# Performance work log

Measured on AMD Instinct MI355X. Metric: run time of the kernel, lower is better.

## Reference

```python
import jax, jax.numpy as jnp
import numpy as np
from jax import lax

B, C, H, W = 32, 64, 56, 56
G = 4            # num_heads*2 with num_heads=2
SMK, K = 5, 7
C2 = C // 2
HEAD_DIM = C // G
SCALE = HEAD_DIM ** -0.5


def _bias_idx(k, h, w):
    # static replica of ContMix.generate_idx + apply_rpb index construction
    rpb_size = 2 * k - 1
    idx_h = np.arange(k)
    idx_w = np.arange(k)
    idx_k = (idx_h[:, None] * rpb_size + idx_w).reshape(-1)
    rep_h = np.ones(k, np.int64); rep_h[k // 2] = h - (k - 1)
    rep_w = np.ones(k, np.int64); rep_w[k // 2] = w - (k - 1)
    bias_hw = np.repeat(idx_h, rep_h)[:, None] * rpb_size + np.repeat(idx_w, rep_w)  # (h, w)
    bias_idx = (bias_hw[..., None] + idx_k).reshape(-1, k * k)[::-1]  # torch.flip dim 0
    return jnp.asarray(bias_idx.copy())

IDX1 = _bias_idx(SMK, H, W)
IDX2 = _bias_idx(K, H, W)


def setup_inputs() -> dict:
    key = jax.random.key(0)
    ks = jax.random.split(key, 18)
    r = lambda i, sh: jax.random.normal(ks[i], sh, jnp.float32)
    return dict(
        x=r(0, (B, C, H, W)),
        lepe_w=r(1, (C, 1, K, K)) * 0.1,
        lepe_b=r(2, (C,)) * 0.1,
        lepe_bn_s=1.0 + 0.1 * r(3, (C,)),
        lepe_bn_b=0.1 * r(4, (C,)),
        wq_w=r(5, (C2, C2)) * (C2 ** -0.5),
        wq_bn_s=1.0 + 0.1 * r(6, (C2,)),
        wq_bn_b=0.1 * r(7, (C2,)),
        wk_w=r(8, (C2, C2)) * (C2 ** -0.5),
        wk_bn_s=1.0 + 0.1 * r(9, (C2,)),
        wk_bn_b=0.1 * r(10, (C2,)),
        wp_w=r(11, (SMK * SMK + K * K, 49)) * (49 ** -0.5),
        wp_b=0.1 * r(12, (SMK * SMK + K * K,)),
        rpb1=0.02 * r(13, (G, 2 * SMK - 1, 2 * SMK - 1)),
        rpb2=0.02 * r(14, (G, 2 * K - 1, 2 * K - 1)),
        dy_w=r(15, (C, C)) * (C ** -0.5),
        dy_bn_s=1.0 + 0.1 * r(16, (C,)),
        dy_bn_b=0.1 * r(17, (C,)),
    )


def _per_ch(t):
    return t[None, :, None, None]


def _contmix(x, lepe_w, lepe_b, lepe_bn_s, lepe_bn_b, wq_w, wq_bn_s, wq_bn_b,
             wk_w, wk_bn_s, wk_bn_b, wp_w, wp_b, rpb1, rpb2, dy_w, dy_bn_s, dy_bn_b):
    # lepe: deploy-mode DilatedReparamBlock = depthwise 7x7 conv (+bias), then eval BN
    lepe = lax.conv_general_dilated(x, lepe_w, (1, 1), [(K // 2, K // 2)] * 2,
                                    feature_group_count=C)
    lepe = (lepe + _per_ch(lepe_b)) * _per_ch(lepe_bn_s) + _per_ch(lepe_bn_b)

    q, kf = jnp.split(x, 2, axis=1)                         # (B, C2, H, W) each
    q = jnp.einsum('oi,bihw->bohw', wq_w, q)                # weight_query 1x1 conv
    q = (q * _per_ch(wq_bn_s) + _per_ch(wq_bn_b)) * SCALE
    # weight_key: AdaptiveAvgPool2d(7) -> 1x1 conv -> BN (H,W divisible by 7)
    kp = kf.reshape(B, C2, 7, H // 7, 7, W // 7).mean(axis=(3, 5))
    kp = jnp.einsum('oi,bihw->bohw', wk_w, kp)
    kp = kp * _per_ch(wk_bn_s) + _per_ch(wk_bn_b)

    qg = q.reshape(B, G, C2 // G, H * W)                    # b g c n
    kg = kp.reshape(B, G, C2 // G, 49)                      # b g c l
    w = jnp.einsum('bgcn,bgcl->bgnl', qg, kg)               # (B, G, HW, 49)
    # weight_proj: 1x1 conv over the 49 pooled-context channels
    w = jnp.einsum('ml,bgnl->bgnm', wp_w, w) + wp_b         # (B, G, HW, 74)
    w = w.reshape(B, G, H, W, SMK * SMK + K * K)

    attn1 = w[..., :SMK * SMK]
    attn2 = w[..., SMK * SMK:]
    attn1 = attn1 + rpb1.reshape(G, -1)[:, IDX1].reshape(1, G, H, W, SMK * SMK)
    attn2 = attn2 + rpb2.reshape(G, -1)[:, IDX2].reshape(1, G, H, W, K * K)
    attn1 = jax.nn.softmax(attn1, axis=-1)
    attn2 = jax.nn.softmax(attn2, axis=-1)

    c = C // (2 * G)                                        # value head dim = 8
    v = x.reshape(B, 2, G, c, H, W)                         # 'b (m g c) h w'

    def dyn_mix(attn, val, k):
        # unfold + einsum: content-adaptive depthwise mixing
        p = lax.conv_general_dilated_patches(
            val.reshape(B, G * c, H, W), (k, k), (1, 1), [(k // 2, k // 2)] * 2,
            dimension_numbers=('NCHW', 'OIHW', 'NCHW'))
        p = p.reshape(B, G, c, k * k, H, W)                 # channel-major patch layout
        return jnp.einsum('bgckhw,bghwk->bgchw', p, attn)

    x1 = dyn_mix(attn1, v[:, 0], SMK)
    x2 = dyn_mix(attn2, v[:, 1], K)
    out = jnp.concatenate([x1, x2], axis=1).reshape(B, C, H, W)
    out = jnp.einsum('oi,bihw->bohw', dy_w, out)            # dyconv_proj 1x1 + BN
    out = out * _per_ch(dy_bn_s) + _per_ch(dy_bn_b)
    return out + lepe


def reference(x, lepe_w, lepe_b, lepe_bn_s, lepe_bn_b, wq_w, wq_bn_s, wq_bn_b,
              wk_w, wk_bn_s, wk_bn_b, wp_w, wp_b, rpb1, rpb2, dy_w, dy_bn_s, dy_bn_b):
    return _contmix(x, lepe_w, lepe_b, lepe_bn_s, lepe_bn_b, wq_w, wq_bn_s, wq_bn_b,
                    wk_w, wk_bn_s, wk_bn_b, wp_w, wp_b, rpb1, rpb2, dy_w, dy_bn_s, dy_bn_b)
```

## Files before the change

### kernel.cpp

```cpp
#include <hip/hip_runtime.h>

#define BB 32
#define CC 64
#define C2 32
#define HH 56
#define WW 56
#define HW 3136

__global__ __launch_bounds__(256) void lepe_k(const float* __restrict__ x,
                                              const float* __restrict__ wt,
                                              const float* __restrict__ b,
                                              const float* __restrict__ s,
                                              const float* __restrict__ bb,
                                              float* __restrict__ out) {
    const int t = blockIdx.x * 256 + threadIdx.x;
    const int q = t % 784;
    const int bc = t / 784;
    const int c = bc & 63;
    const int r = q / 14;
    const int c4 = (q % 14) * 4;
    const float* xp = x + (long)bc * HW;
    float acc0 = 0.f, acc1 = 0.f, acc2 = 0.f, acc3 = 0.f;
    #pragma unroll
    for (int i = 0; i < 7; ++i) {
        const int y = r + i - 3;
        if ((unsigned)y >= HH) continue;
        float w7[7];
        #pragma unroll
        for (int j = 0; j < 7; ++j) w7[j] = wt[c * 49 + i * 7 + j];
        const float4* row = reinterpret_cast<const float4*>(xp + y * WW + c4 - 4);
        float4 A = make_float4(0.f, 0.f, 0.f, 0.f);
        float4 Cv = make_float4(0.f, 0.f, 0.f, 0.f);
        if (c4 != 0) A = row[0];
        const float4 Bv = row[1];
        if (c4 != 52) Cv = row[2];
        const float w12[12] = {A.x, A.y, A.z, A.w, Bv.x, Bv.y, Bv.z, Bv.w, Cv.x, Cv.y, Cv.z, Cv.w};
        #pragma unroll
        for (int j = 0; j < 7; ++j) {
            acc0 = fmaf(w12[j + 1], w7[j], acc0);
            acc1 = fmaf(w12[j + 2], w7[j], acc1);
            acc2 = fmaf(w12[j + 3], w7[j], acc2);
            acc3 = fmaf(w12[j + 4], w7[j], acc3);
        }
    }
    const float bc_ = b[c], sc = s[c], bbc = bb[c];
    float* op = out + (long)bc * HW + r * WW + c4;
    op[0] = (acc0 + bc_) * sc + bbc;
    op[1] = (acc1 + bc_) * sc + bbc;
    op[2] = (acc2 + bc_) * sc + bbc;
    op[3] = (acc3 + bc_) * sc + bbc;
}

__global__ __launch_bounds__(256) void q_k(const float* __restrict__ x,
                                           const float* __restrict__ wq,
                                           const float* __restrict__ s,
                                           const float* __restrict__ bb,
                                           float* __restrict__ q) {
    __shared__ float wsm[32 * 32];
    const int b = blockIdx.y;
    const int tid = threadIdx.x;
    for (int i = tid; i < 1024; i += 256) wsm[(i & 31) * 32 + (i >> 5)] = wq[i];
    __syncthreads();
    const int n = blockIdx.x * 256 + tid;
    if (n >= HW) return;
    const float* xp = x + (long)b * CC * HW;
    float acc[32];
    #pragma unroll
    for (int o = 0; o < 32; ++o) acc[o] = 0.f;
    for (int i = 0; i < 32; ++i) {
        const float xv = xp[i * HW + n];
        #pragma unroll
        for (int o = 0; o < 32; ++o) acc[o] = fmaf(wsm[i * 32 + o], xv, acc[o]);
    }
    float* qp = q + (long)b * C2 * HW + n;
    #pragma unroll
    for (int o = 0; o < 32; ++o)
        qp[o * HW] = (acc[o] * s[o] + bb[o]) * 0.25f;
}

__global__ __launch_bounds__(256) void prep_k(const float* __restrict__ x,
                                              const float* __restrict__ wk,
                                              const float* __restrict__ wks,
                                              const float* __restrict__ wkb,
                                              const float* __restrict__ wp_w,
                                              float* __restrict__ WK) {
    __shared__ float p_s[32 * 49];
    __shared__ float kg_s[8 * 49];
    const int b = blockIdx.x >> 2;
    const int g = blockIdx.x & 3;
    const int tid = threadIdx.x;
    for (int idx = tid; idx < 1568; idx += 256) {
        const int i = idx / 49, l = idx % 49;
        const int py = l / 7, px = l % 7;
        const float4* xp4 = reinterpret_cast<const float4*>(
            x + ((long)(b * CC + 32 + i)) * HW + py * 8 * WW + px * 8);
        float4 sA = make_float4(0.f, 0.f, 0.f, 0.f);
        float4 sB = make_float4(0.f, 0.f, 0.f, 0.f);
        #pragma unroll
        for (int y = 0; y < 8; ++y) {
            const float4 a = xp4[y * 14];
            const float4 c = xp4[y * 14 + 1];
            sA.x += a.x; sA.y += a.y; sA.z += a.z; sA.w += a.w;
            sB.x += c.x; sB.y += c.y; sB.z += c.z; sB.w += c.w;
        }
        p_s[idx] = (sA.x + sA.y + sA.z + sA.w + sB.x + sB.y + sB.z + sB.w) * (1.f / 64.f);
    }
    __syncthreads();
    for (int idx = tid; idx < 392; idx += 256) {
        const int o8 = idx / 49, l = idx % 49;
        const int o = g * 8 + o8;
        float acc = 0.f;
        #pragma unroll
        for (int i = 0; i < 32; ++i) acc = fmaf(wk[o * 32 + i], p_s[i * 49 + l], acc);
        kg_s[idx] = acc * wks[o] + wkb[o];
    }
    __syncthreads();
    for (int idx = tid; idx < 640; idx += 256) {
        const int c = idx / 80, slot = idx % 80;
        float acc = 0.f;
        int m = -1;
        if (slot < 28) { if (slot < 25) m = slot; }
        else           { if (slot < 77) m = 25 + (slot - 28); }
        if (m >= 0) {
            const float* kp = kg_s + c * 49;
            #pragma unroll
            for (int l = 0; l < 49; ++l) acc = fmaf(wp_w[m * 49 + l], kp[l], acc);
        }
        const long base = (long)blockIdx.x * 640;
        if (slot < 28) WK[base + c * 28 + slot] = acc;
        else           WK[base + 224 + c * 52 + (slot - 28)] = acc;
    }
}

__global__ __launch_bounds__(256) void attnmix_k(const float* __restrict__ x,
                                                 const float* __restrict__ q,
                                                 const float* __restrict__ WK,
                                                 const float* __restrict__ wp_b,
                                                 const float* __restrict__ rpb1,
                                                 const float* __restrict__ rpb2,
                                                 float* __restrict__ mix) {
    __shared__ float WK1_s[8 * 28];
    __shared__ float WK2_s[8 * 52];
    __shared__ float wpb1_s[25];
    __shared__ float wpb2_s[49];
    __shared__ float rpb1_s[81];
    __shared__ float rpb2_s[169];
    const int tid = threadIdx.x;
    const int bg = blockIdx.y;
    const int g = bg & 3, b = bg >> 2;
    {
        const float* wkp = WK + (long)bg * 640;
        for (int i = tid; i < 224; i += 256) WK1_s[i] = wkp[i];
        for (int i = tid; i < 416; i += 256) WK2_s[i] = wkp[224 + i];
    }
    if (tid < 25) wpb1_s[tid] = wp_b[tid];
    if (tid >= 32 && tid < 81) wpb2_s[tid - 32] = wp_b[25 + tid - 32];
    if (tid < 81) rpb1_s[tid] = rpb1[g * 81 + tid];
    if (tid < 169) rpb2_s[tid] = rpb2[g * 169 + tid];
    __syncthreads();
    const int n = blockIdx.x * 256 + tid;
    if (n >= HW) return;

    const int ph = n / WW, pw = n % WW;
    const int yr = HH - 1 - ph, xr = WW - 1 - pw;

    float q8[8];
    #pragma unroll
    for (int c = 0; c < 8; ++c) q8[c] = q[((long)b * C2 + g * 8 + c) * HW + n];

    {
        float w1[25];
        #pragma unroll
        for (int m = 0; m < 25; ++m) w1[m] = wpb1_s[m];
        #pragma unroll
        for (int c = 0; c < 8; ++c) {
            const float qv = q8[c];
            #pragma unroll
            for (int m = 0; m < 25; ++m) w1[m] = fmaf(qv, WK1_s[c * 28 + m], w1[m]);
        }
        const int rh5 = yr < 2 ? yr : (yr > 53 ? yr - 51 : 2);
        const int rw5 = xr < 2 ? xr : (xr > 53 ? xr - 51 : 2);
        #pragma unroll
        for (int i = 0; i < 5; ++i)
            #pragma unroll
            for (int j = 0; j < 5; ++j)
                w1[i * 5 + j] += rpb1_s[(rh5 + i) * 9 + (rw5 + j)];
        float mx = -1e30f;
        #pragma unroll
        for (int m = 0; m < 25; ++m) mx = fmaxf(mx, w1[m]);
        float sm = 0.f;
        #pragma unroll
        for (int m = 0; m < 25; ++m) { w1[m] = __expf(w1[m] - mx); sm += w1[m]; }
        const float r = 1.f / sm;
        #pragma unroll
        for (int m = 0; m < 25; ++m) w1[m] *= r;

        const float* vb = x + ((long)b * CC + g * 8) * HW + n;
        float acc[8];
        #pragma unroll
        for (int ch = 0; ch < 8; ++ch) acc[ch] = 0.f;
        #pragma unroll
        for (int i = 0; i < 5; ++i) {
            const int y = ph + i - 2;
            if ((unsigned)y >= HH) continue;
            #pragma unroll
            for (int j = 0; j < 5; ++j) {
                const int xx = pw + j - 2;
                if ((unsigned)xx >= WW) continue;
                const int off = (i - 2) * WW + (j - 2);
                const float wv = w1[i * 5 + j];
                #pragma unroll
                for (int ch = 0; ch < 8; ++ch)
                    acc[ch] = fmaf(wv, vb[ch * HW + off], acc[ch]);
            }
        }
        float* m0 = mix + ((long)b * CC + g * 8) * HW + n;
        #pragma unroll
        for (int ch = 0; ch < 8; ++ch) m0[ch * HW] = acc[ch];
    }

    __builtin_amdgcn_sched_barrier(0);

    {
        float w2[49];
        #pragma unroll
        for (int m = 0; m < 49; ++m) w2[m] = wpb2_s[m];
        #pragma unroll
        for (int c = 0; c < 8; ++c) {
            const float qv = q8[c];
            #pragma unroll
            for (int m = 0; m < 49; ++m) w2[m] = fmaf(qv, WK2_s[c * 52 + m], w2[m]);
        }
        const int rh7 = yr < 3 ? yr : (yr > 52 ? yr - 49 : 3);
        const int rw7 = xr < 3 ? xr : (xr > 52 ? xr - 49 : 3);
        #pragma unroll
        for (int i = 0; i < 7; ++i)
            #pragma unroll
            for (int j = 0; j < 7; ++j)
                w2[i * 7 + j] += rpb2_s[(rh7 + i) * 13 + (rw7 + j)];
        float mx = -1e30f;
        #pragma unroll
        for (int m = 0; m < 49; ++m) mx = fmaxf(mx, w2[m]);
        float sm = 0.f;
        #pragma unroll
        for (int m = 0; m < 49; ++m) { w2[m] = __expf(w2[m] - mx); sm += w2[m]; }
        const float r = 1.f / sm;
        #pragma unroll
        for (int m = 0; m < 49; ++m) w2[m] *= r;

        const float* vb = x + ((long)b * CC + 32 + g * 8) * HW + n;
        float acc[8];
        #pragma unroll
        for (int ch = 0; ch < 8; ++ch) acc[ch] = 0.f;
        #pragma unroll
        for (int i = 0; i < 7; ++i) {
            const int y = ph + i - 3;
            if ((unsigned)y >= HH) continue;
            #pragma unroll
            for (int j = 0; j < 7; ++j) {
                const int xx = pw + j - 3;
                if ((unsigned)xx >= WW) continue;
                const int off = (i - 3) * WW + (j - 3);
                const float wv = w2[i * 7 + j];
                #pragma unroll
                for (int ch = 0; ch < 8; ++ch)
                    acc[ch] = fmaf(wv, vb[ch * HW + off], acc[ch]);
            }
        }
        float* m1 = mix + ((long)b * CC + 32 + g * 8) * HW + n;
        #pragma unroll
        for (int ch = 0; ch < 8; ++ch) m1[ch * HW] = acc[ch];
    }
}

__global__ __launch_bounds__(256) void final_k(const float* __restrict__ mix,
                                               const float* __restrict__ dy_w,
                                               const float* __restrict__ s,
                                               const float* __restrict__ bb,
                                               float* __restrict__ out) {
    __shared__ float w_s[64 * 64];
    const int tid = threadIdx.x;
    const int b = blockIdx.y;
    for (int i = tid; i < 4096; i += 256) w_s[(i & 63) * 64 + (i >> 6)] = dy_w[i];
    __syncthreads();
    const int ob = (tid >> 7) * 32;
    const int p2 = blockIdx.x * 128 + (tid & 127);
    if (p2 >= 1568) return;
    const float2* mp = reinterpret_cast<const float2*>(mix + (long)b * CC * HW);
    float accx[32], accy[32];
    #pragma unroll
    for (int o = 0; o < 32; ++o) { accx[o] = 0.f; accy[o] = 0.f; }
    for (int i = 0; i < 64; ++i) {
        const float2 mv = mp[i * 1568 + p2];
        const float* wr = w_s + i * 64 + ob;
        #pragma unroll
        for (int o = 0; o < 32; ++o) {
            const float wv = wr[o];
            accx[o] = fmaf(wv, mv.x, accx[o]);
            accy[o] = fmaf(wv, mv.y, accy[o]);
        }
    }
    float2* op = reinterpret_cast<float2*>(out + (long)b * CC * HW);
    #pragma unroll
    for (int o = 0; o < 32; ++o) {
        const long idx = (long)(ob + o) * 1568 + p2;
        const float2 prev = op[idx];
        float2 res;
        res.x = fmaf(accx[o], s[ob + o], bb[ob + o]) + prev.x;
        res.y = fmaf(accy[o], s[ob + o], bb[ob + o]) + prev.y;
        op[idx] = res;
    }
}

extern "C" void kernel_launch(void* const* d_in, const int* in_sizes, int n_in,
                              void* d_out, int out_size, void* d_ws, size_t ws_size,
                              hipStream_t stream) {
    const float* x       = (const float*)d_in[0];
    const float* lepe_w  = (const float*)d_in[1];
    const float* lepe_b  = (const float*)d_in[2];
    const float* lepe_s  = (const float*)d_in[3];
    const float* lepe_bb = (const float*)d_in[4];
    const float* wq_w    = (const float*)d_in[5];
    const float* wq_s    = (const float*)d_in[6];
    const float* wq_bb   = (const float*)d_in[7];
    const float* wk_w    = (const float*)d_in[8];
    const float* wk_s    = (const float*)d_in[9];
    const float* wk_bb   = (const float*)d_in[10];
    const float* wp_w    = (const float*)d_in[11];
    const float* wp_b    = (const float*)d_in[12];
    const float* rpb1    = (const float*)d_in[13];
    const float* rpb2    = (const float*)d_in[14];
    const float* dy_w    = (const float*)d_in[15];
    const float* dy_s    = (const float*)d_in[16];
    const float* dy_bb   = (const float*)d_in[17];
    float* out = (float*)d_out;

    float* ws     = (float*)d_ws;
    float* q_ws   = ws;
    float* WK_ws  = q_ws + 32 * 32 * HW;
    float* mix_ws = WK_ws + 128 * 640;

    const int nTiles = (HW + 255) / 256;

    lepe_k<<<dim3(2048 * 784 / 256), 256, 0, stream>>>(x, lepe_w, lepe_b, lepe_s, lepe_bb, out);
    q_k<<<dim3(nTiles, BB), 256, 0, stream>>>(x, wq_w, wq_s, wq_bb, q_ws);
    prep_k<<<dim3(BB * 4), 256, 0, stream>>>(x, wk_w, wk_s, wk_bb, wp_w, WK_ws);
    attnmix_k<<<dim3(nTiles, BB * 4), 256, 0, stream>>>(x, q_ws, WK_ws, wp_b, rpb1, rpb2, mix_ws);
    final_k<<<dim3(13, BB), 256, 0, stream>>>(mix_ws, dy_w, dy_s, dy_bb, out);
}
```

Baseline: 271.8 us.

## Fuse q projection, dynamic mixing and output projection into one kernel

Replaces the separate q_k, attnmix_k and final_k kernels with a single mega_k. Each thread computes q, both softmax attention mixes and the 64-channel output projection for all four groups of one pixel, keeping the accumulators in registers. This removes the q and mix workspace round-trips through global memory and two launches. The grid shrinks to 13x32 blocks with a very large register footprint (64 accumulators plus 49 weights), so low occupancy and possible spills could hurt. The lepe kernel also now stages its 49 weights in shared memory and uses a 2D grid.

```diff
diff --git a/kernel.cpp b/kernel.cpp
--- a/kernel.cpp
+++ b/kernel.cpp
@@ -13,21 +13,22 @@
                                               const float* __restrict__ s,
                                               const float* __restrict__ bb,
                                               float* __restrict__ out) {
-    const int t = blockIdx.x * 256 + threadIdx.x;
-    const int q = t % 784;
-    const int bc = t / 784;
+    __shared__ float w_s[49];
+    const int bc = blockIdx.y;
     const int c = bc & 63;
-    const int r = q / 14;
-    const int c4 = (q % 14) * 4;
+    const int tid = threadIdx.x;
+    if (tid < 49) w_s[tid] = wt[c * 49 + tid];
+    __syncthreads();
+    const int qi = blockIdx.x * 256 + tid;
+    if (qi >= 784) return;
+    const int r = qi / 14;
+    const int c4 = (qi % 14) * 4;
     const float* xp = x + (long)bc * HW;
     float acc0 = 0.f, acc1 = 0.f, acc2 = 0.f, acc3 = 0.f;
     #pragma unroll
     for (int i = 0; i < 7; ++i) {
         const int y = r + i - 3;
         if ((unsigned)y >= HH) continue;
-        float w7[7];
-        #pragma unroll
-        for (int j = 0; j < 7; ++j) w7[j] = wt[c * 49 + i * 7 + j];
         const float4* row = reinterpret_cast<const float4*>(xp + y * WW + c4 - 4);
         float4 A = make_float4(0.f, 0.f, 0.f, 0.f);
         float4 Cv = make_float4(0.f, 0.f, 0.f, 0.f);
@@ -37,10 +38,11 @@
         const float w12[12] = {A.x, A.y, A.z, A.w, Bv.x, Bv.y, Bv.z, Bv.w, Cv.x, Cv.y, Cv.z, Cv.w};
         #pragma unroll
         for (int j = 0; j < 7; ++j) {
-            acc0 = fmaf(w12[j + 1], w7[j], acc0);
-            acc1 = fmaf(w12[j + 2], w7[j], acc1);
-            acc2 = fmaf(w12[j + 3], w7[j], acc2);
-            acc3 = fmaf(w12[j + 4], w7[j], acc3);
+            const float wv = w_s[i * 7 + j];
+            acc0 = fmaf(w12[j + 1], wv, acc0);
+            acc1 = fmaf(w12[j + 2], wv, acc1);
+            acc2 = fmaf(w12[j + 3], wv, acc2);
+            acc3 = fmaf(w12[j + 4], wv, acc3);
         }
     }
     const float bc_ = b[c], sc = s[c], bbc = bb[c];
@@ -49,33 +51,6 @@
     op[1] = (acc1 + bc_) * sc + bbc;
     op[2] = (acc2 + bc_) * sc + bbc;
     op[3] = (acc3 + bc_) * sc + bbc;
-}
-
-__global__ __launch_bounds__(256) void q_k(const float* __restrict__ x,
-                                           const float* __restrict__ wq,
-                                           const float* __restrict__ s,
-                                           const float* __restrict__ bb,
-                                           float* __restrict__ q) {
-    __shared__ float wsm[32 * 32];
-    const int b = blockIdx.y;
-    const int tid = threadIdx.x;
-    for (int i = tid; i < 1024; i += 256) wsm[(i & 31) * 32 + (i >> 5)] = wq[i];
-    __syncthreads();
-    const int n = blockIdx.x * 256 + tid;
-    if (n >= HW) return;
-    const float* xp = x + (long)b * CC * HW;
-    float acc[32];
-    #pragma unroll
-    for (int o = 0; o < 32; ++o) acc[o] = 0.f;
-    for (int i = 0; i < 32; ++i) {
-        const float xv = xp[i * HW + n];
-        #pragma unroll
-        for (int o = 0; o < 32; ++o) acc[o] = fmaf(wsm[i * 32 + o], xv, acc[o]);
-    }
-    float* qp = q + (long)b * C2 * HW + n;
-    #pragma unroll
-    for (int o = 0; o < 32; ++o)
-        qp[o * HW] = (acc[o] * s[o] + bb[o]) * 0.25f;
 }
 
 __global__ __launch_bounds__(256) void prep_k(const float* __restrict__ x,
@@ -132,184 +107,196 @@
     }
 }
 
-__global__ __launch_bounds__(256) void attnmix_k(const float* __restrict__ x,
-                                                 const float* __restrict__ q,
-                                                 const float* __restrict__ WK,
-                                                 const float* __restrict__ wp_b,
-                                                 const float* __restrict__ rpb1,
-                                                 const float* __restrict__ rpb2,
-                                                 float* __restrict__ mix) {
-    __shared__ float WK1_s[8 * 28];
-    __shared__ float WK2_s[8 * 52];
+__global__ __launch_bounds__(256) void mega_k(const float* __restrict__ x,
+                                              const float* __restrict__ WK,
+                                              const float* __restrict__ wq_w,
+                                              const float* __restrict__ wq_s,
+                                              const float* __restrict__ wq_bb,
+                                              const float* __restrict__ wp_b,
+                                              const float* __restrict__ rpb1,
+                                              const float* __restrict__ rpb2,
+                                              const float* __restrict__ dy_w,
+                                              const float* __restrict__ dy_s,
+                                              const float* __restrict__ dy_bb,
+                                              float* __restrict__ out) {
+    __shared__ float wqT_s[32 * 32];
+    __shared__ float dyT_s[64 * 64];
+    __shared__ float WK_s[2560];
+    __shared__ float rpb1_s[324];
+    __shared__ float rpb2_s[676];
     __shared__ float wpb1_s[25];
     __shared__ float wpb2_s[49];
-    __shared__ float rpb1_s[81];
-    __shared__ float rpb2_s[169];
+    __shared__ float wqbn_s[64];
+    __shared__ float dybn_s[128];
     const int tid = threadIdx.x;
-    const int bg = blockIdx.y;
-    const int g = bg & 3, b = bg >> 2;
+    const int b = blockIdx.y;
+    for (int i = tid; i < 1024; i += 256) wqT_s[(i & 31) * 32 + (i >> 5)] = wq_w[i];
+    for (int i = tid; i < 4096; i += 256) dyT_s[(i & 63) * 64 + (i >> 6)] = dy_w[i];
     {
-        const float* wkp = WK + (long)bg * 640;
-        for (int i = tid; i < 224; i += 256) WK1_s[i] = wkp[i];
-        for (int i = tid; i < 416; i += 256) WK2_s[i] = wkp[224 + i];
-    }
+        const float* wkp = WK + (long)b * 2560;
+        for (int i = tid; i < 2560; i += 256) WK_s[i] = wkp[i];
+    }
+    for (int i = tid; i < 324; i += 256) rpb1_s[i] = rpb1[i];
+    for (int i = tid; i < 676; i += 256) rpb2_s[i] = rpb2[i];
     if (tid < 25) wpb1_s[tid] = wp_b[tid];
-    if (tid >= 32 && tid < 81) wpb2_s[tid - 32] = wp_b[25 + tid - 32];
-    if (tid < 81) rpb1_s[tid] = rpb1[g * 81 + tid];
-    if (tid < 169) rpb2_s[tid] = rpb2[g * 169 + tid];
+    if (tid >= 64 && tid < 113) wpb2_s[tid - 64] = wp_b[25 + tid - 64];
+    if (tid < 32) wqbn_s[tid] = wq_s[tid];
+    if (tid >= 32 && tid < 64) wqbn_s[tid] = wq_bb[tid - 32];
+    if (tid < 64) dybn_s[tid] = dy_s[tid];
+    if (tid >= 64 && tid < 128) dybn_s[tid] = dy_bb[tid - 64];
     __syncthreads();
     const int n = blockIdx.x * 256 + tid;
     if (n >= HW) return;
 
     const int ph = n / WW, pw = n % WW;
     const int yr = HH - 1 - ph, xr = WW - 1 - pw;
-
-    float q8[8];
+    const int rh5 = yr < 2 ? yr : (yr > 53 ? yr - 51 : 2);
+    const int rw5 = xr < 2 ? xr : (xr > 53 ? xr - 51 : 2);
+    const int rh7 = yr < 3 ? yr : (yr > 52 ? yr - 49 : 3);
+    const int rw7 = xr < 3 ? xr : (xr > 52 ? xr - 49 : 3);
+
+    const float* xb = x + (long)b * CC * HW + n;
+    float* op = out + (long)b * CC * HW + n;
+
+    float out64[64];
     #pragma unroll
-    for (int c = 0; c < 8; ++c) q8[c] = q[((long)b * C2 + g * 8 + c) * HW + n];
-
-    {
-        float w1[25];
-        #pragma unroll
-        for (int m = 0; m < 25; ++m) w1[m] = wpb1_s[m];
-        #pragma unroll
-        for (int c = 0; c < 8; ++c) {
-            const float qv = q8[c];
-            #pragma unroll
-            for (int m = 0; m < 25; ++m) w1[m] = fmaf(qv, WK1_s[c * 28 + m], w1[m]);
-        }
-        const int rh5 = yr < 2 ? yr : (yr > 53 ? yr - 51 : 2);
-        const int rw5 = xr < 2 ? xr : (xr > 53 ? xr - 51 : 2);
-        #pragma unroll
-        for (int i = 0; i < 5; ++i)
-            #pragma unroll
-            for (int j = 0; j < 5; ++j)
-                w1[i * 5 + j] += rpb1_s[(rh5 + i) * 9 + (rw5 + j)];
-        float mx = -1e30f;
-        #pragma unroll
-        for (int m = 0; m < 25; ++m) mx = fmaxf(mx, w1[m]);
-        float sm = 0.f;
-        #pragma unroll
-        for (int m = 0; m < 25; ++m) { w1[m] = __expf(w1[m] - mx); sm += w1[m]; }
-        const float r = 1.f / sm;
-        #pragma unroll
-        for (int m = 0; m < 25; ++m) w1[m] *= r;
-
-        const float* vb = x + ((long)b * CC + g * 8) * HW + n;
-        float acc[8];
-        #pragma unroll
-        for (int ch = 0; ch < 8; ++ch) acc[ch] = 0.f;
-        #pragma unroll
-        for (int i = 0; i < 5; ++i) {
-            const int y = ph + i - 2;
-            if ((unsigned)y >= HH) continue;
-            #pragma unroll
-            for (int j = 0; j < 5; ++j) {
-                const int xx = pw + j - 2;
-                if ((unsigned)xx >= WW) continue;
-                const int off = (i - 2) * WW + (j - 2);
-                const float wv = w1[i * 5 + j];
-                #pragma unroll
-                for (int ch = 0; ch < 8; ++ch)
-                    acc[ch] = fmaf(wv, vb[ch * HW + off], acc[ch]);
-            }
-        }
-        float* m0 = mix + ((long)b * CC + g * 8) * HW + n;
-        #pragma unroll
-        for (int ch = 0; ch < 8; ++ch) m0[ch * HW] = acc[ch];
-    }
-
-    __builtin_amdgcn_sched_barrier(0);
-
-    {
-        float w2[49];
-        #pragma unroll
-        for (int m = 0; m < 49; ++m) w2[m] = wpb2_s[m];
-        #pragma unroll
-        for (int c = 0; c < 8; ++c) {
-            const float qv = q8[c];
-            #pragma unroll
-            for (int m = 0; m < 49; ++m) w2[m] = fmaf(qv, WK2_s[c * 52 + m], w2[m]);
-        }
-        const int rh7 = yr < 3 ? yr : (yr > 52 ? yr - 49 : 3);
-        const int rw7 = xr < 3 ? xr : (xr > 52 ? xr - 49 : 3);
-        #pragma unroll
-        for (int i = 0; i < 7; ++i)
-            #pragma unroll
-            for (int j = 0; j < 7; ++j)
-                w2[i * 7 + j] += rpb2_s[(rh7 + i) * 13 + (rw7 + j)];
-        float mx = -1e30f;
-        #pragma unroll
-        for (int m = 0; m < 49; ++m) mx = fmaxf(mx, w2[m]);
-        float sm = 0.f;
-        #pragma unroll
-        for (int m = 0; m < 49; ++m) { w2[m] = __expf(w2[m] - mx); sm += w2[m]; }
-        const float r = 1.f / sm;
-        #pragma unroll
-        for (int m = 0; m < 49; ++m) w2[m] *= r;
-
-        const float* vb = x + ((long)b * CC + 32 + g * 8) * HW + n;
-        float acc[8];
-        #pragma unroll
-        for (int ch = 0; ch < 8; ++ch) acc[ch] = 0.f;
-        #pragma unroll
-        for (int i = 0; i < 7; ++i) {
-            const int y = ph + i - 3;
-            if ((unsigned)y >= HH) continue;
-            #pragma unroll
-            for (int j = 0; j < 7; ++j) {
-                const int xx = pw + j - 3;
-                if ((unsigned)xx >= WW) continue;
-                const int off = (i - 3) * WW + (j - 3);
-                const float wv = w2[i * 7 + j];
-                #pragma unroll
-                for (int ch = 0; ch < 8; ++ch)
-                    acc[ch] = fmaf(wv, vb[ch * HW + off], acc[ch]);
-            }
-        }
-        float* m1 = mix + ((long)b * CC + 32 + g * 8) * HW + n;
-        #pragma unroll
-        for (int ch = 0; ch < 8; ++ch) m1[ch * HW] = acc[ch];
-    }
-}
-
-__global__ __launch_bounds__(256) void final_k(const float* __restrict__ mix,
-                                               const float* __restrict__ dy_w,
-                                               const float* __restrict__ s,
-                                               const float* __restrict__ bb,
-                                               float* __restrict__ out) {
-    __shared__ float w_s[64 * 64];
-    const int tid = threadIdx.x;
-    const int b = blockIdx.y;
-    for (int i = tid; i < 4096; i += 256) w_s[(i & 63) * 64 + (i >> 6)] = dy_w[i];
-    __syncthreads();
-    const int ob = (tid >> 7) * 32;
-    const int p2 = blockIdx.x * 128 + (tid & 127);
-    if (p2 >= 1568) return;
-    const float2* mp = reinterpret_cast<const float2*>(mix + (long)b * CC * HW);
-    float accx[32], accy[32];
+    for (int o = 0; o < 64; ++o) out64[o] = 0.f;
+
+    #pragma unroll 1
+    for (int g = 0; g < 4; ++g) {
+        float q8[8];
+        #pragma unroll
+        for (int c = 0; c < 8; ++c) q8[c] = 0.f;
+        for (int i = 0; i < 32; ++i) {
+            const float xv = xb[i * HW];
+            #pragma unroll
+            for (int c = 0; c < 8; ++c)
+                q8[c] = fmaf(wqT_s[i * 32 + g * 8 + c], xv, q8[c]);
+        }
+        #pragma unroll
+        for (int c = 0; c < 8; ++c)
+            q8[c] = (q8[c] * wqbn_s[g * 8 + c] + wqbn_s[32 + g * 8 + c]) * 0.25f;
+
+        __builtin_amdgcn_sched_barrier(0);
+
+        {
+            const float* wk1 = WK_s + g * 640;
+            float w1[25];
+            #pragma unroll
+            for (int m = 0; m < 25; ++m) w1[m] = wpb1_s[m];
+            #pragma unroll
+            for (int c = 0; c < 8; ++c) {
+                const float qv = q8[c];
+                #pragma unroll
+                for (int m = 0; m < 25; ++m) w1[m] = fmaf(qv, wk1[c * 28 + m], w1[m]);
+            }
+            const float* rp = rpb1_s + g * 81;
+            #pragma unroll
+            for (int i = 0; i < 5; ++i)
+                #pragma unroll
+                for (int j = 0; j < 5; ++j)
+                    w1[i * 5 + j] += rp[(rh5 + i) * 9 + (rw5 + j)];
+            float mx = -1e30f;
+            #pragma unroll
+            for (int m = 0; m < 25; ++m) mx = fmaxf(mx, w1[m]);
+            float sm = 0.f;
+            #pragma unroll
+            for (int m = 0; m < 25; ++m) { w1[m] = __expf(w1[m] - mx); sm += w1[m]; }
+            const float r = 1.f / sm;
+            #pragma unroll
+            for (int m = 0; m < 25; ++m) w1[m] *= r;
+
+            const float* vb = xb + (long)(g * 8) * HW;
+            float acc[8];
+            #pragma unroll
+            for (int ch = 0; ch < 8; ++ch) acc[ch] = 0.f;
+            #pragma unroll
+            for (int i = 0; i < 5; ++i) {
+                const int y = ph + i - 2;
+                if ((unsigned)y >= HH) continue;
+                #pragma unroll
+                for (int j = 0; j < 5; ++j) {
+                    const int xx = pw + j - 2;
+                    if ((unsigned)xx >= WW) continue;
+                    const int off = (i - 2) * WW + (j - 2);
+                    const float wv = w1[i * 5 + j];
+                    #pragma unroll
+                    for (int ch = 0; ch < 8; ++ch)
+                        acc[ch] = fmaf(wv, vb[ch * HW + off], acc[ch]);
+                }
+            }
+            #pragma unroll
+            for (int c = 0; c < 8; ++c) {
+                const float mv = acc[c];
+                const float* dr = dyT_s + (g * 8 + c) * 64;
+                #pragma unroll
+                for (int o = 0; o < 64; ++o) out64[o] = fmaf(dr[o], mv, out64[o]);
+            }
+        }
+
+        __builtin_amdgcn_sched_barrier(0);
+
+        {
+            const float* wk2 = WK_s + g * 640 + 224;
+            float w2[49];
+            #pragma unroll
+            for (int m = 0; m < 49; ++m) w2[m] = wpb2_s[m];
+            #pragma unroll
+            for (int c = 0; c < 8; ++c) {
+                const float qv = q8[c];
+                #pragma unroll
+                for (int m = 0; m < 49; ++m) w2[m] = fmaf(qv, wk2[c * 52 + m], w2[m]);
+            }
+            const float* rp = rpb2_s + g * 169;
+            #pragma unroll
+            for (int i = 0; i < 7; ++i)
+                #pragma unroll
+                for (int j = 0; j < 7; ++j)
+                    w2[i * 7 + j] += rp[(rh7 + i) * 13 + (rw7 + j)];
+            float mx = -1e30f;
+            #pragma unroll
+            for (int m = 0; m < 49; ++m) mx = fmaxf(mx, w2[m]);
+            float sm = 0.f;
+            #pragma unroll
+            for (int m = 0; m < 49; ++m) { w2[m] = __expf(w2[m] - mx); sm += w2[m]; }
+            const float r = 1.f / sm;
+            #pragma unroll
+            for (int m = 0; m < 49; ++m) w2[m] *= r;
+
+            const float* vb = xb + (long)(32 + g * 8) * HW;
+            float acc[8];
+            #pragma unroll
+            for (int ch = 0; ch < 8; ++ch) acc[ch] = 0.f;
+            #pragma unroll
+            for (int i = 0; i < 7; ++i) {
+                const int y = ph + i - 3;
+                if ((unsigned)y >= HH) continue;
+                #pragma unroll
+                for (int j = 0; j < 7; ++j) {
+                    const int xx = pw + j - 3;
+                    if ((unsigned)xx >= WW) continue;
+                    const int off = (i - 3) * WW + (j - 3);
+                    const float wv = w2[i * 7 + j];
+                    #pragma unroll
+                    for (int ch = 0; ch < 8; ++ch)
+                        acc[ch] = fmaf(wv, vb[ch * HW + off], acc[ch]);
+                }
+            }
+            #pragma unroll
+            for (int c = 0; c < 8; ++c) {
+                const float mv = acc[c];
+                const float* dr = dyT_s + (32 + g * 8 + c) * 64;
+                #pragma unroll
+                for (int o = 0; o < 64; ++o) out64[o] = fmaf(dr[o], mv, out64[o]);
+            }
+        }
+
+        __builtin_amdgcn_sched_barrier(0);
+    }
+
     #pragma unroll
-    for (int o = 0; o < 32; ++o) { accx[o] = 0.f; accy[o] = 0.f; }
-    for (int i = 0; i < 64; ++i) {
-        const float2 mv = mp[i * 1568 + p2];
-        const float* wr = w_s + i * 64 + ob;
-        #pragma unroll
-        for (int o = 0; o < 32; ++o) {
-            const float wv = wr[o];
-            accx[o] = fmaf(wv, mv.x, accx[o]);
-            accy[o] = fmaf(wv, mv.y, accy[o]);
-        }
-    }
-    float2* op = reinterpret_cast<float2*>(out + (long)b * CC * HW);
-    #pragma unroll
-    for (int o = 0; o < 32; ++o) {
-        const long idx = (long)(ob + o) * 1568 + p2;
-        const float2 prev = op[idx];
-        float2 res;
-        res.x = fmaf(accx[o], s[ob + o], bb[ob + o]) + prev.x;
-        res.y = fmaf(accy[o], s[ob + o], bb[ob + o]) + prev.y;
-        op[idx] = res;
-    }
+    for (int o = 0; o < 64; ++o)
+        op[o * HW] = fmaf(out64[o], dybn_s[o], dybn_s[64 + o]) + op[o * HW];
 }
 
 extern "C" void kernel_launch(void* const* d_in, const int* in_sizes, int n_in,
@@ -335,16 +322,10 @@
     const float* dy_bb   = (const float*)d_in[17];
     float* out = (float*)d_out;
 
-    float* ws     = (float*)d_ws;
-    float* q_ws   = ws;
-    float* WK_ws  = q_ws + 32 * 32 * HW;
-    float* mix_ws = WK_ws + 128 * 640;
-
-    const int nTiles = (HW + 255) / 256;
-
-    lepe_k<<<dim3(2048 * 784 / 256), 256, 0, stream>>>(x, lepe_w, lepe_b, lepe_s, lepe_bb, out);
-    q_k<<<dim3(nTiles, BB), 256, 0, stream>>>(x, wq_w, wq_s, wq_bb, q_ws);
+    float* WK_ws = (float*)d_ws;
+
+    lepe_k<<<dim3(4, BB * CC), 256, 0, stream>>>(x, lepe_w, lepe_b, lepe_s, lepe_bb, out);
     prep_k<<<dim3(BB * 4), 256, 0, stream>>>(x, wk_w, wk_s, wk_bb, wp_w, WK_ws);
-    attnmix_k<<<dim3(nTiles, BB * 4), 256, 0, stream>>>(x, q_ws, WK_ws, wp_b, rpb1, rpb2, mix_ws);
-    final_k<<<dim3(13, BB), 256, 0, stream>>>(mix_ws, dy_w, dy_s, dy_bb, out);
+    mega_k<<<dim3(13, BB), 256, 0, stream>>>(x, WK_ws, wq_w, wq_s, wq_bb, wp_b,
+                                             rpb1, rpb2, dy_w, dy_s, dy_bb, out);
 }
```

Result: slower. 586.1 us (+115.6%).

## Fuse q projection into attnmix, stage lepe weights in LDS, split final_k outputs

Applied to the files above, without the earlier changes.

Removes the separate q_k kernel and its q workspace round-trip; each attnmix block now computes its 8 q channels from x using a transposed wq slice held in shared memory. The lepe kernel is regridded to one channel-image per block row so the 49 taps are loaded once into shared memory. final_k halves the output channels per thread to 16 and doubles its grid, cutting register pressure and raising parallelism. The price is redundant q compute: each of the 4 groups re-reads 32 x channels, and lepe blocks have idle tail threads.

```diff
diff --git a/kernel.cpp b/kernel.cpp
--- a/kernel.cpp
+++ b/kernel.cpp
@@ -13,21 +13,22 @@
                                               const float* __restrict__ s,
                                               const float* __restrict__ bb,
                                               float* __restrict__ out) {
-    const int t = blockIdx.x * 256 + threadIdx.x;
-    const int q = t % 784;
-    const int bc = t / 784;
+    __shared__ float w_s[49];
+    const int bc = blockIdx.y;
     const int c = bc & 63;
-    const int r = q / 14;
-    const int c4 = (q % 14) * 4;
+    const int tid = threadIdx.x;
+    if (tid < 49) w_s[tid] = wt[c * 49 + tid];
+    __syncthreads();
+    const int qi = blockIdx.x * 256 + tid;
+    if (qi >= 784) return;
+    const int r = qi / 14;
+    const int c4 = (qi % 14) * 4;
     const float* xp = x + (long)bc * HW;
     float acc0 = 0.f, acc1 = 0.f, acc2 = 0.f, acc3 = 0.f;
     #pragma unroll
     for (int i = 0; i < 7; ++i) {
         const int y = r + i - 3;
         if ((unsigned)y >= HH) continue;
-        float w7[7];
-        #pragma unroll
-        for (int j = 0; j < 7; ++j) w7[j] = wt[c * 49 + i * 7 + j];
         const float4* row = reinterpret_cast<const float4*>(xp + y * WW + c4 - 4);
         float4 A = make_float4(0.f, 0.f, 0.f, 0.f);
         float4 Cv = make_float4(0.f, 0.f, 0.f, 0.f);
@@ -37,10 +38,11 @@
         const float w12[12] = {A.x, A.y, A.z, A.w, Bv.x, Bv.y, Bv.z, Bv.w, Cv.x, Cv.y, Cv.z, Cv.w};
         #pragma unroll
         for (int j = 0; j < 7; ++j) {
-            acc0 = fmaf(w12[j + 1], w7[j], acc0);
-            acc1 = fmaf(w12[j + 2], w7[j], acc1);
-            acc2 = fmaf(w12[j + 3], w7[j], acc2);
-            acc3 = fmaf(w12[j + 4], w7[j], acc3);
+            const float wv = w_s[i * 7 + j];
+            acc0 = fmaf(w12[j + 1], wv, acc0);
+            acc1 = fmaf(w12[j + 2], wv, acc1);
+            acc2 = fmaf(w12[j + 3], wv, acc2);
+            acc3 = fmaf(w12[j + 4], wv, acc3);
         }
     }
     const float bc_ = b[c], sc = s[c], bbc = bb[c];
@@ -49,33 +51,6 @@
     op[1] = (acc1 + bc_) * sc + bbc;
     op[2] = (acc2 + bc_) * sc + bbc;
     op[3] = (acc3 + bc_) * sc + bbc;
-}
-
-__global__ __launch_bounds__(256) void q_k(const float* __restrict__ x,
-                                           const float* __restrict__ wq,
-                                           const float* __restrict__ s,
-                                           const float* __restrict__ bb,
-                                           float* __restrict__ q) {
-    __shared__ float wsm[32 * 32];
-    const int b = blockIdx.y;
-    const int tid = threadIdx.x;
-    for (int i = tid; i < 1024; i += 256) wsm[(i & 31) * 32 + (i >> 5)] = wq[i];
-    __syncthreads();
-    const int n = blockIdx.x * 256 + tid;
-    if (n >= HW) return;
-    const float* xp = x + (long)b * CC * HW;
-    float acc[32];
-    #pragma unroll
-    for (int o = 0; o < 32; ++o) acc[o] = 0.f;
-    for (int i = 0; i < 32; ++i) {
-        const float xv = xp[i * HW + n];
-        #pragma unroll
-        for (int o = 0; o < 32; ++o) acc[o] = fmaf(wsm[i * 32 + o], xv, acc[o]);
-    }
-    float* qp = q + (long)b * C2 * HW + n;
-    #pragma unroll
-    for (int o = 0; o < 32; ++o)
-        qp[o * HW] = (acc[o] * s[o] + bb[o]) * 0.25f;
 }
 
 __global__ __launch_bounds__(256) void prep_k(const float* __restrict__ x,
@@ -133,18 +108,22 @@
 }
 
 __global__ __launch_bounds__(256) void attnmix_k(const float* __restrict__ x,
-                                                 const float* __restrict__ q,
                                                  const float* __restrict__ WK,
+                                                 const float* __restrict__ wq_w,
+                                                 const float* __restrict__ wq_s,
+                                                 const float* __restrict__ wq_bb,
                                                  const float* __restrict__ wp_b,
                                                  const float* __restrict__ rpb1,
                                                  const float* __restrict__ rpb2,
                                                  float* __restrict__ mix) {
     __shared__ float WK1_s[8 * 28];
     __shared__ float WK2_s[8 * 52];
+    __shared__ float wqT_s[32 * 8];
     __shared__ float wpb1_s[25];
     __shared__ float wpb2_s[49];
     __shared__ float rpb1_s[81];
     __shared__ float rpb2_s[169];
+    __shared__ float wqbn_s[16];
     const int tid = threadIdx.x;
     const int bg = blockIdx.y;
     const int g = bg & 3, b = bg >> 2;
@@ -153,10 +132,16 @@
         for (int i = tid; i < 224; i += 256) WK1_s[i] = wkp[i];
         for (int i = tid; i < 416; i += 256) WK2_s[i] = wkp[224 + i];
     }
+    if (tid < 256) {
+        const int i = tid >> 3, c = tid & 7;
+        wqT_s[tid] = wq_w[(g * 8 + c) * 32 + i];
+    }
     if (tid < 25) wpb1_s[tid] = wp_b[tid];
     if (tid >= 32 && tid < 81) wpb2_s[tid - 32] = wp_b[25 + tid - 32];
     if (tid < 81) rpb1_s[tid] = rpb1[g * 81 + tid];
     if (tid < 169) rpb2_s[tid] = rpb2[g * 169 + tid];
+    if (tid >= 192 && tid < 200) wqbn_s[tid - 192] = wq_s[g * 8 + tid - 192];
+    if (tid >= 200 && tid < 208) wqbn_s[8 + tid - 200] = wq_bb[g * 8 + tid - 200];
     __syncthreads();
     const int n = blockIdx.x * 256 + tid;
     if (n >= HW) return;
@@ -164,9 +149,21 @@
     const int ph = n / WW, pw = n % WW;
     const int yr = HH - 1 - ph, xr = WW - 1 - pw;
 
+    const float* xb = x + (long)b * CC * HW + n;
+
     float q8[8];
     #pragma unroll
-    for (int c = 0; c < 8; ++c) q8[c] = q[((long)b * C2 + g * 8 + c) * HW + n];
+    for (int c = 0; c < 8; ++c) q8[c] = 0.f;
+    for (int i = 0; i < 32; ++i) {
+        const float xv = xb[i * HW];
+        #pragma unroll
+        for (int c = 0; c < 8; ++c) q8[c] = fmaf(wqT_s[i * 8 + c], xv, q8[c]);
+    }
+    #pragma unroll
+    for (int c = 0; c < 8; ++c)
+        q8[c] = (q8[c] * wqbn_s[c] + wqbn_s[8 + c]) * 0.25f;
+
+    __builtin_amdgcn_sched_barrier(0);
 
     {
         float w1[25];
@@ -195,7 +192,7 @@
         #pragma unroll
         for (int m = 0; m < 25; ++m) w1[m] *= r;
 
-        const float* vb = x + ((long)b * CC + g * 8) * HW + n;
+        const float* vb = xb + (long)(g * 8) * HW;
         float acc[8];
         #pragma unroll
         for (int ch = 0; ch < 8; ++ch) acc[ch] = 0.f;
@@ -248,7 +245,7 @@
         #pragma unroll
         for (int m = 0; m < 49; ++m) w2[m] *= r;
 
-        const float* vb = x + ((long)b * CC + 32 + g * 8) * HW + n;
+        const float* vb = xb + (long)(32 + g * 8) * HW;
         float acc[8];
         #pragma unroll
         for (int ch = 0; ch < 8; ++ch) acc[ch] = 0.f;
@@ -283,18 +280,18 @@
     const int b = blockIdx.y;
     for (int i = tid; i < 4096; i += 256) w_s[(i & 63) * 64 + (i >> 6)] = dy_w[i];
     __syncthreads();
-    const int ob = (tid >> 7) * 32;
-    const int p2 = blockIdx.x * 128 + (tid & 127);
+    const int ob = (tid >> 6) * 16;
+    const int p2 = blockIdx.x * 64 + (tid & 63);
     if (p2 >= 1568) return;
     const float2* mp = reinterpret_cast<const float2*>(mix + (long)b * CC * HW);
-    float accx[32], accy[32];
-    #pragma unroll
-    for (int o = 0; o < 32; ++o) { accx[o] = 0.f; accy[o] = 0.f; }
+    float accx[16], accy[16];
+    #pragma unroll
+    for (int o = 0; o < 16; ++o) { accx[o] = 0.f; accy[o] = 0.f; }
     for (int i = 0; i < 64; ++i) {
         const float2 mv = mp[i * 1568 + p2];
         const float* wr = w_s + i * 64 + ob;
         #pragma unroll
-        for (int o = 0; o < 32; ++o) {
+        for (int o = 0; o < 16; ++o) {
             const float wv = wr[o];
             accx[o] = fmaf(wv, mv.x, accx[o]);
             accy[o] = fmaf(wv, mv.y, accy[o]);
@@ -302,7 +299,7 @@
     }
     float2* op = reinterpret_cast<float2*>(out + (long)b * CC * HW);
     #pragma unroll
-    for (int o = 0; o < 32; ++o) {
+    for (int o = 0; o < 16; ++o) {
         const long idx = (long)(ob + o) * 1568 + p2;
         const float2 prev = op[idx];
         float2 res;
@@ -336,15 +333,14 @@
     float* out = (float*)d_out;
 
     float* ws     = (float*)d_ws;
-    float* q_ws   = ws;
-    float* WK_ws  = q_ws + 32 * 32 * HW;
+    float* WK_ws  = ws;
     float* mix_ws = WK_ws + 128 * 640;
 
     const int nTiles = (HW + 255) / 256;
 
-    lepe_k<<<dim3(2048 * 784 / 256), 256, 0, stream>>>(x, lepe_w, lepe_b, lepe_s, lepe_bb, out);
-    q_k<<<dim3(nTiles, BB), 256, 0, stream>>>(x, wq_w, wq_s, wq_bb, q_ws);
+    lepe_k<<<dim3(4, BB * CC), 256, 0, stream>>>(x, lepe_w, lepe_b, lepe_s, lepe_bb, out);
     prep_k<<<dim3(BB * 4), 256, 0, stream>>>(x, wk_w, wk_s, wk_bb, wp_w, WK_ws);
-    attnmix_k<<<dim3(nTiles, BB * 4), 256, 0, stream>>>(x, q_ws, WK_ws, wp_b, rpb1, rpb2, mix_ws);
-    final_k<<<dim3(13, BB), 256, 0, stream>>>(mix_ws, dy_w, dy_s, dy_bb, out);
-}
+    attnmix_k<<<dim3(nTiles, BB * 4), 256, 0, stream>>>(x, WK_ws, wq_w, wq_s, wq_bb,
+                                                        wp_b, rpb1, rpb2, mix_ws);
+    final_k<<<dim3(25, BB), 256, 0, stream>>>(mix_ws, dy_w, dy_s, dy_bb, out);
+}
```

Measured after the change: 256.1 us. -5.8%, faster.
